# Kernel tuning notes

Hardware: AMD Instinct MI355X
Metric: run time of the kernel (lower is better)

## Reference

```python
import jax, jax.numpy as jnp
import numpy as np

B, S, D, L, R = 8, 128, 512, 512, 50  # batch, seq_len, input_dim, linear_dim, n_rel_labels


def _head_params(key, n_out):
    k1, k2, k3, k4 = jax.random.split(key, 4)
    s1 = 1.0 / np.sqrt(2 * D)
    s2 = 1.0 / np.sqrt(L)
    return (jax.random.uniform(k1, (2 * D, L), jnp.float32, -s1, s1),
            jax.random.uniform(k2, (L,), jnp.float32, -s1, s1),
            jax.random.uniform(k3, (L, n_out), jnp.float32, -s2, s2),
            jax.random.uniform(k4, (n_out,), jnp.float32, -s2, s2))


def setup_inputs() -> dict:
    key = jax.random.key(0)
    kx, ks, kh, kt, kl = jax.random.split(key, 5)
    x = jax.random.normal(kx, (B, S, D), jnp.float32)
    span = _head_params(ks, 1)
    h2h = _head_params(kh, 1)
    t2t = _head_params(kt, 1)
    lab = _head_params(kl, R)
    return {
        'x': x,
        'span_W1': span[0], 'span_b1': span[1], 'span_W2': span[2], 'span_b2': span[3],
        'h2h_W1': h2h[0], 'h2h_b1': h2h[1], 'h2h_W2': h2h[2], 'h2h_b2': h2h[3],
        't2t_W1': t2t[0], 't2t_b1': t2t[1], 't2t_W2': t2t[2], 't2t_b2': t2t[3],
        'lab_W1': lab[0], 'lab_b1': lab[1], 'lab_W2': lab[2], 'lab_b2': lab[3],
    }


def _pair_head(x, W1, b1, W2, b2):
    # Linear on concat([x_i, x_j]) == x_i @ W_left + x_j @ W_right  (avoids [B,S,S,2D] concat)
    d = x.shape[-1]
    Wl, Wr = W1[:d], W1[d:]
    left = jnp.einsum('bid,dl->bil', x, Wl)   # [B,S,L]
    right = jnp.einsum('bjd,dl->bjl', x, Wr)  # [B,S,L]
    h = jnp.tanh(left[:, :, None, :] + right[:, None, :, :] + b1)  # [B,S,S,L]
    return jnp.einsum('bijl,lo->bijo', h, W2) + b2  # [B,S,S,n_out]


def reference(x, span_W1, span_b1, span_W2, span_b2,
              h2h_W1, h2h_b1, h2h_W2, h2h_b2,
              t2t_W1, t2t_b1, t2t_W2, t2t_b2,
              lab_W1, lab_b1, lab_W2, lab_b2):
    shst = _pair_head(x, span_W1, span_b1, span_W2, span_b2)[..., 0]  # [B,S,S]
    # torch: movedim(-1,1) -> triu + triu(1).T -> movedim(1,-1)
    bt = jnp.swapaxes(shst, 1, 2)
    sym = jnp.triu(bt) + jnp.swapaxes(jnp.triu(bt, 1), -1, -2)
    shst = jnp.swapaxes(sym, 1, 2)
    shoh = _pair_head(x, h2h_W1, h2h_b1, h2h_W2, h2h_b2)[..., 0]
    stot = _pair_head(x, t2t_W1, t2t_b1, t2t_W2, t2t_b2)[..., 0]
    shoh_labels = _pair_head(x, lab_W1, lab_b1, lab_W2, lab_b2)  # [B,S,S,R]
    return (shst, shoh, stot, shoh_labels)
```

## Files before the change

### kernel.cpp

```cpp
#include <hip/hip_runtime.h>

#define Bsz 8
#define Ssz 128
#define Dsz 512
#define D2 1024
#define Lsz 512
#define Rsz 50
#define SLOT 524288
#define OUTMAT 131072

typedef __attribute__((ext_vector_type(8))) _Float16 f16x8;
typedef __attribute__((ext_vector_type(2))) __fp16 fp16x2;
typedef __attribute__((ext_vector_type(4))) float f32x4;

union UV4 { uint4 u; f16x8 h; };
union UH { unsigned short s; _Float16 h; };
union UP { fp16x2 h; unsigned u; };

struct K1Args {
  const float* W1[4];
  const float* b1[4];
};

__device__ __forceinline__ unsigned pkrtz(float a, float b) {
  UP c; c.h = __builtin_amdgcn_cvt_pkrtz(a, b); return c.u;
}
__device__ __forceinline__ unsigned short f2h(float v) {
  UH x; x.h = (_Float16)v; return x.s;
}
__device__ __forceinline__ float rcpf(float x) {
  return __builtin_amdgcn_rcpf(x);
}

__device__ __forceinline__ unsigned tanh2u(unsigned ea, unsigned eb) {
  UP a, b, p; a.u = ea; b.u = eb;
  const fp16x2 one = {(__fp16)1.0f, (__fp16)1.0f};
  p.h = a.h * b.h + one;
  const float h0 = fmaf(-2.0f, rcpf((float)p.h.x), 1.0f);
  const float h1 = fmaf(-2.0f, rcpf((float)p.h.y), 1.0f);
  return pkrtz(h0, h1);
}

__device__ __forceinline__ float d2(unsigned a, unsigned b, unsigned w,
                                    float acc) {
  UP pa, pb, pw, ps; pa.u = a; pb.u = b; pw.u = w;
  const fp16x2 one = {(__fp16)1.0f, (__fp16)1.0f};
  fp16x2 p = pa.h * pb.h + one;
  ps.u = pkrtz(rcpf((float)p.x), rcpf((float)p.y));
  return __builtin_amdgcn_fdot2(ps.h, pw.h, acc, false);
}

__global__ __launch_bounds__(256) void prep_all(
    const float* __restrict__ x, K1Args a, const float* __restrict__ W2,
    const float* __restrict__ w2a, const float* __restrict__ w2b,
    const float* __restrict__ w2c,
    const float* __restrict__ b2a, const float* __restrict__ b2b,
    const float* __restrict__ b2c,
    unsigned short* __restrict__ W1F, unsigned short* __restrict__ X16F,
    unsigned short* __restrict__ W2F, float* __restrict__ Sums) {
  const int z = blockIdx.z;
  const int t = threadIdx.x;
  if (z < 4) {
    if (blockIdx.x >= 8) return;
    __shared__ float S[64][65];
    const float* __restrict__ W = a.W1[z];
    const int n0 = blockIdx.x * 64;
    const int k0 = blockIdx.y * 64;
    {
      const int kk = t >> 2, c16 = (t & 3) * 16;
      const float* p = W + (k0 + kk) * Lsz + n0 + c16;
#pragma unroll
      for (int c = 0; c < 4; ++c) {
        float4 v = *(const float4*)(p + c * 4);
        S[kk][c16 + c * 4 + 0] = v.x; S[kk][c16 + c * 4 + 1] = v.y;
        S[kk][c16 + c * 4 + 2] = v.z; S[kk][c16 + c * 4 + 3] = v.w;
      }
    }
    __syncthreads();
#pragma unroll
    for (int o = t; o < 512; o += 256) {
      const int lane = o & 63;
      const int ntl = (o >> 6) & 3, kbl = o >> 8;
      const int n_l = ntl * 16 + (lane & 15);
      const int k_l = kbl * 32 + (lane >> 4) * 8;
      uint4 pk;
      pk.x = pkrtz(S[k_l + 0][n_l], S[k_l + 1][n_l]);
      pk.y = pkrtz(S[k_l + 2][n_l], S[k_l + 3][n_l]);
      pk.z = pkrtz(S[k_l + 4][n_l], S[k_l + 5][n_l]);
      pk.w = pkrtz(S[k_l + 6][n_l], S[k_l + 7][n_l]);
      const long addr =
          ((long)((z * 32 + blockIdx.x * 4 + ntl) * 32 + blockIdx.y * 2 + kbl) *
               64 + lane) * 8;
      *(uint4*)(W1F + addr) = pk;
    }
  } else if (z == 4) {
    if (blockIdx.x >= 16) return;
    const int idx = (blockIdx.y * 16 + blockIdx.x) * 256 + t;
    const int frag = idx >> 6, lane = idx & 63;
    const int m = (frag >> 4) * 16 + (lane & 15);
    const int k0 = (frag & 15) * 32 + (lane >> 4) * 8;
    const float* p = x + m * Dsz + k0;
    float4 v0 = *(const float4*)p, v1 = *(const float4*)(p + 4);
    uint4 pk = make_uint4(pkrtz(v0.x, v0.y), pkrtz(v0.z, v0.w),
                          pkrtz(v1.x, v1.y), pkrtz(v1.z, v1.w));
    *(uint4*)(X16F + (long)idx * 8) = pk;
  } else {
    if (blockIdx.y != 0) return;
    if (blockIdx.x < 16) {
      const int idx = blockIdx.x * 256 + t;
      const int frag = idx >> 6, lane = idx & 63;
      const int o = (frag >> 4) * 16 + (lane & 15);
      const int k0 = (frag & 15) * 32 + (lane >> 4) * 8;
      float v[8];
#pragma unroll
      for (int e = 0; e < 8; ++e)
        v[e] = (o < Rsz) ? W2[(k0 + e) * Rsz + o] : 0.0f;
      uint4 pk = make_uint4(pkrtz(v[0], v[1]), pkrtz(v[2], v[3]),
                            pkrtz(v[4], v[5]), pkrtz(v[6], v[7]));
      *(uint4*)(W2F + (long)idx * 8) = pk;
    } else if (blockIdx.x < 19) {
      const int h = blockIdx.x - 16;
      const float* __restrict__ w2 = (h == 0) ? w2a : (h == 1 ? w2b : w2c);
      const float bb = (h == 0) ? b2a[0] : (h == 1 ? b2b[0] : b2c[0]);
      __shared__ float red[256];
      red[t] = w2[t] + w2[t + 256];
      __syncthreads();
      for (int s = 128; s > 0; s >>= 1) {
        if (t < s) red[t] += red[t + s];
        __syncthreads();
      }
      if (t == 0) Sums[h] = red[0] + bb;
    }
  }
}

__global__ __launch_bounds__(256) void gemm_lr_f16f(
    const unsigned short* __restrict__ X16F,
    const unsigned short* __restrict__ W1F, K1Args a,
    unsigned short* __restrict__ U) {
  const int side = blockIdx.z;
  const int h = side >> 1, r = side & 1;
  const float* __restrict__ bias = a.b1[h];
  const int tid = threadIdx.x;
  const int w = tid >> 6, lane = tid & 63;
  const int lm = lane & 15, q = lane >> 4;
  const int mtb = blockIdx.y * 4 + (w & 1) * 2;
  const int ntb = blockIdx.x * 4 + (w >> 1) * 2;

  f32x4 acc[2][2];
#pragma unroll
  for (int mt = 0; mt < 2; ++mt)
#pragma unroll
    for (int nt = 0; nt < 2; ++nt) {
      acc[mt][nt].x = 0.f; acc[mt][nt].y = 0.f;
      acc[mt][nt].z = 0.f; acc[mt][nt].w = 0.f;
    }

  for (int kb = 0; kb < 16; ++kb) {
    UV4 af[2], bf[2];
#pragma unroll
    for (int mt = 0; mt < 2; ++mt)
      af[mt].u = *(const uint4*)(X16F +
          ((long)((mtb + mt) * 16 + kb) * 64 + lane) * 8);
#pragma unroll
    for (int nt = 0; nt < 2; ++nt)
      bf[nt].u = *(const uint4*)(W1F +
          ((long)((h * 32 + ntb + nt) * 32 + r * 16 + kb) * 64 + lane) * 8);
#pragma unroll
    for (int mt = 0; mt < 2; ++mt)
#pragma unroll
      for (int nt = 0; nt < 2; ++nt)
        acc[mt][nt] = __builtin_amdgcn_mfma_f32_16x16x32_f16(
            af[mt].h, bf[nt].h, acc[mt][nt], 0, 0, 0);
  }

  unsigned short* slot = U + side * SLOT;
#pragma unroll
  for (int nt = 0; nt < 2; ++nt) {
    const int n_out = (ntb + nt) * 16 + lm;
    const float bb = (r == 0) ? bias[n_out] : 0.0f;
#pragma unroll
    for (int mt = 0; mt < 2; ++mt) {
#pragma unroll
      for (int reg = 0; reg < 4; ++reg) {
        const int m_out = (mtb + mt) * 16 + q * 4 + reg;
        float v;
        if (reg == 0) v = acc[mt][nt].x;
        else if (reg == 1) v = acc[mt][nt].y;
        else if (reg == 2) v = acc[mt][nt].z;
        else v = acc[mt][nt].w;
        slot[m_out * Lsz + n_out] = f2h(__expf(2.0f * (v + bb)));
      }
    }
  }
}

__global__ __launch_bounds__(256) void pair_fused(
    const unsigned short* __restrict__ U,
    const unsigned short* __restrict__ W2F,
    const float* __restrict__ b2l,
    const float* __restrict__ w2a, const float* __restrict__ w2b,
    const float* __restrict__ w2c, const float* __restrict__ Sums,
    float* __restrict__ out) {
  __shared__ unsigned short As[2][16][68];
  __shared__ unsigned short Bs[2][32][68];
  __shared__ unsigned w2p[2][32];

  const int b = blockIdx.y;
  const int tid = threadIdx.x;
  const int w = tid >> 6, lane = tid & 63;
  const int lm = lane & 15, q = lane >> 4;

  if ((blockIdx.x & 1) == 0) {
    const int i = blockIdx.x >> 1;
    const int jb = w * 32;

    const unsigned short* __restrict__ Lrow =
        U + 6 * SLOT + (b * Ssz + i) * Lsz;
    const unsigned short* __restrict__ Rb0 = U + 7 * SLOT + (long)b * Ssz * Lsz;
    float* out3 = out + 3 * OUTMAT;

    const unsigned short* Lb = Lrow + q * 8;
    const unsigned short* R0 = Rb0 + (jb + lm) * Lsz + q * 8;
    const unsigned short* R1 = Rb0 + (jb + 16 + lm) * Lsz + q * 8;
    const unsigned short* Bb = W2F + lane * 8;

    f32x4 acc[2][4];
#pragma unroll
    for (int mt = 0; mt < 2; ++mt)
#pragma unroll
      for (int nt = 0; nt < 4; ++nt) {
        acc[mt][nt].x = 0.f; acc[mt][nt].y = 0.f;
        acc[mt][nt].z = 0.f; acc[mt][nt].w = 0.f;
      }

#pragma unroll 2
    for (int c = 0; c < 8; ++c) {
      const uint4 lf0 = *(const uint4*)(Lb + c * 64);
      const uint4 lf1 = *(const uint4*)(Lb + c * 64 + 32);
#pragma unroll
      for (int kbl = 0; kbl < 2; ++kbl) {
        const uint4 lf = kbl ? lf1 : lf0;
        UV4 bfr[4];
#pragma unroll
        for (int nt = 0; nt < 4; ++nt)
          bfr[nt].u =
              *(const uint4*)(Bb + (long)(nt * 16 + kbl + 2 * c) * 512);
#pragma unroll
        for (int mt = 0; mt < 2; ++mt) {
          const uint4 rv =
              *(const uint4*)((mt ? R1 : R0) + c * 64 + kbl * 32);
          UV4 A;
          A.u = make_uint4(tanh2u(lf.x, rv.x), tanh2u(lf.y, rv.y),
                           tanh2u(lf.z, rv.z), tanh2u(lf.w, rv.w));
#pragma unroll
          for (int nt = 0; nt < 4; ++nt)
            acc[mt][nt] = __builtin_amdgcn_mfma_f32_16x16x32_f16(
                A.h, bfr[nt].h, acc[mt][nt], 0, 0, 0);
        }
      }
    }

#pragma unroll
    for (int nt = 0; nt < 4; ++nt) {
      const int o = nt * 16 + lm;
      if (o >= Rsz) continue;
      const float bias = b2l[o];
#pragma unroll
      for (int mt = 0; mt < 2; ++mt) {
#pragma unroll
        for (int reg = 0; reg < 4; ++reg) {
          const int j = jb + mt * 16 + q * 4 + reg;
          const long base = ((long)((b * Ssz + i) * Ssz) + j) * Rsz;
          float v;
          if (reg == 0) v = acc[mt][nt].x;
          else if (reg == 1) v = acc[mt][nt].y;
          else if (reg == 2) v = acc[mt][nt].z;
          else v = acc[mt][nt].w;
          out3[base + o] = v + bias;
        }
      }
    }
  } else {
    const int s = blockIdx.x >> 1;
    if (s >= 96) return;
    const int h = s >> 5;
    const int r = s & 31;
    const int it = r >> 2, jt = r & 3;
    const int i0 = it * 16, j0 = jt * 32;
    if (h == 0 && i0 + 15 < j0) return;
    const int t = tid;
    const int tj = t & 31;
    const int th = t >> 5;
    const int iA = th * 2;

    const unsigned short* __restrict__ A =
        U + (2 * h) * SLOT + (long)(b * Ssz + i0) * Lsz;
    const unsigned short* __restrict__ Bt =
        U + (2 * h + 1) * SLOT + (long)(b * Ssz + j0) * Lsz;
    const float* __restrict__ w2 = (h == 0) ? w2a : (h == 1 ? w2b : w2c);

    const int srow = t >> 3;
    const int scol = (t & 7) * 8;
    const unsigned short* Ag = A + srow * Lsz + scol;
    const unsigned short* Bg = Bt + srow * Lsz + scol;

    float accA0 = 0.f, accB0 = 0.f, accA1 = 0.f, accB1 = 0.f;

    {
      uint4 ra, rb; unsigned rw = 0;
      if (t < 128) ra = *(const uint4*)(Ag);
      rb = *(const uint4*)(Bg);
      if (t < 32) rw = pkrtz(w2[2 * t], w2[2 * t + 1]);
      if (t < 128) *(uint4*)&As[0][srow][scol] = ra;
      *(uint4*)&Bs[0][srow][scol] = rb;
      if (t < 32) w2p[0][t] = rw;
    }
    __syncthreads();

#pragma unroll 1
    for (int c = 0; c < 8; ++c) {
      const int buf = c & 1;
      uint4 ra, rb; unsigned rw = 0;
      if (c < 7) {
        const int lc = (c + 1) * 64;
        if (t < 128) ra = *(const uint4*)(Ag + lc);
        rb = *(const uint4*)(Bg + lc);
        if (t < 32) rw = pkrtz(w2[lc + 2 * t], w2[lc + 2 * t + 1]);
      }
#pragma unroll
      for (int l = 0; l < 64; l += 4) {
        const uint2 av0 = *(const uint2*)&As[buf][iA][l];
        const uint2 av1 = *(const uint2*)&As[buf][iA + 1][l];
        const uint2 bv  = *(const uint2*)&Bs[buf][tj][l];
        const unsigned w0 = w2p[buf][l >> 1];
        const unsigned w1 = w2p[buf][(l >> 1) + 1];
        accA0 = d2(av0.x, bv.x, w0, accA0);
        accB0 = d2(av0.y, bv.y, w1, accB0);
        accA1 = d2(av1.x, bv.x, w0, accA1);
        accB1 = d2(av1.y, bv.y, w1, accB1);
      }
      if (c < 7) {
        const int nb = buf ^ 1;
        if (t < 128) *(uint4*)&As[nb][srow][scol] = ra;
        *(uint4*)&Bs[nb][srow][scol] = rb;
        if (t < 32) w2p[nb][t] = rw;
        __syncthreads();
      }
    }

    const float Sh = Sums[h];
    const float v0 = fmaf(-2.0f, accA0 + accB0, Sh);
    const float v1 = fmaf(-2.0f, accA1 + accB1, Sh);
    const int i = i0 + iA, j = j0 + tj;
    if (h == 0) {
      if (j <= i) {
        out[(b * Ssz + i) * Ssz + j] = v0;
        out[(b * Ssz + j) * Ssz + i] = v0;
      }
      if (j <= i + 1) {
        out[(b * Ssz + i + 1) * Ssz + j] = v1;
        out[(b * Ssz + j) * Ssz + (i + 1)] = v1;
      }
    } else {
      float* o = out + h * OUTMAT;
      o[(b * Ssz + i) * Ssz + j] = v0;
      o[(b * Ssz + i + 1) * Ssz + j] = v1;
    }
  }
}

extern "C" void kernel_launch(void* const* d_in, const int* in_sizes, int n_in,
                              void* d_out, int out_size, void* d_ws,
                              size_t ws_size, hipStream_t stream) {
  (void)in_sizes; (void)n_in; (void)out_size; (void)ws_size;
  const float* x = (const float*)d_in[0];
  K1Args a;
  a.W1[0] = (const float*)d_in[1];  a.b1[0] = (const float*)d_in[2];
  a.W1[1] = (const float*)d_in[5];  a.b1[1] = (const float*)d_in[6];
  a.W1[2] = (const float*)d_in[9];  a.b1[2] = (const float*)d_in[10];
  a.W1[3] = (const float*)d_in[13]; a.b1[3] = (const float*)d_in[14];
  const float* w2a = (const float*)d_in[3];
  const float* b2a = (const float*)d_in[4];
  const float* w2b = (const float*)d_in[7];
  const float* b2b = (const float*)d_in[8];
  const float* w2c = (const float*)d_in[11];
  const float* b2c = (const float*)d_in[12];
  const float* W2l = (const float*)d_in[15];
  const float* b2l = (const float*)d_in[16];
  float* out = (float*)d_out;

  unsigned short* U    = (unsigned short*)d_ws;
  unsigned short* W1F  = U + 8 * SLOT;
  unsigned short* X16F = U + 8 * SLOT + 4 * (Lsz * D2);
  unsigned short* W2F  = U + 8 * SLOT + 5 * (Lsz * D2);
  float* Sums = (float*)(W2F + 64 * Lsz);

  prep_all<<<dim3(19, 16, 6), 256, 0, stream>>>(
      x, a, W2l, w2a, w2b, w2c, b2a, b2b, b2c, W1F, X16F, W2F, Sums);
  gemm_lr_f16f<<<dim3(8, 16, 8), 256, 0, stream>>>(X16F, W1F, a, U);
  pair_fused<<<dim3(256, Bsz), 256, 0, stream>>>(
      U, W2F, b2l, w2a, w2b, w2c, Sums, out);
}
```

Before: 174.5 us.

## Split scalar pair heads over L into four atomic partials and use fp32 math

```diff
diff --git a/kernel.cpp b/kernel.cpp
--- a/kernel.cpp
+++ b/kernel.cpp
@@ -22,6 +22,12 @@
   const float* b1[4];
 };
 
+__device__ __forceinline__ float f16lo(unsigned u) {
+  UH x; x.s = (unsigned short)(u & 0xffffu); return (float)x.h;
+}
+__device__ __forceinline__ float f16hi(unsigned u) {
+  UH x; x.s = (unsigned short)(u >> 16); return (float)x.h;
+}
 __device__ __forceinline__ unsigned pkrtz(float a, float b) {
   UP c; c.h = __builtin_amdgcn_cvt_pkrtz(a, b); return c.u;
 }
@@ -41,15 +47,6 @@
   return pkrtz(h0, h1);
 }
 
-__device__ __forceinline__ float d2(unsigned a, unsigned b, unsigned w,
-                                    float acc) {
-  UP pa, pb, pw, ps; pa.u = a; pb.u = b; pw.u = w;
-  const fp16x2 one = {(__fp16)1.0f, (__fp16)1.0f};
-  fp16x2 p = pa.h * pb.h + one;
-  ps.u = pkrtz(rcpf((float)p.x), rcpf((float)p.y));
-  return __builtin_amdgcn_fdot2(ps.h, pw.h, acc, false);
-}
-
 __global__ __launch_bounds__(256) void prep_all(
     const float* __restrict__ x, K1Args a, const float* __restrict__ W2,
     const float* __restrict__ w2a, const float* __restrict__ w2b,
@@ -57,7 +54,8 @@
     const float* __restrict__ b2a, const float* __restrict__ b2b,
     const float* __restrict__ b2c,
     unsigned short* __restrict__ W1F, unsigned short* __restrict__ X16F,
-    unsigned short* __restrict__ W2F, float* __restrict__ Sums) {
+    unsigned short* __restrict__ W2F, float* __restrict__ Sums,
+    float* __restrict__ out) {
   const int z = blockIdx.z;
   const int t = threadIdx.x;
   if (z < 4) {
@@ -130,6 +128,13 @@
         __syncthreads();
       }
       if (t == 0) Sums[h] = red[0] + bb;
+    } else if (blockIdx.x < 43) {
+      const int zb = blockIdx.x - 19;
+      float* base = out + zb * 16384;
+      const float4 zz = make_float4(0.f, 0.f, 0.f, 0.f);
+#pragma unroll
+      for (int k = 0; k < 16; ++k)
+        *(float4*)(base + k * 1024 + t * 4) = zz;
     }
   }
 }
@@ -202,17 +207,18 @@
     const float* __restrict__ w2a, const float* __restrict__ w2b,
     const float* __restrict__ w2c, const float* __restrict__ Sums,
     float* __restrict__ out) {
-  __shared__ unsigned short As[2][16][68];
-  __shared__ unsigned short Bs[2][32][68];
-  __shared__ unsigned w2p[2][32];
+  __shared__ unsigned short As[16][66];
+  __shared__ unsigned short Bs[32][66];
+  __shared__ float w2s[64];
 
   const int b = blockIdx.y;
   const int tid = threadIdx.x;
-  const int w = tid >> 6, lane = tid & 63;
-  const int lm = lane & 15, q = lane >> 4;
-
-  if ((blockIdx.x & 1) == 0) {
-    const int i = blockIdx.x >> 1;
+  const int xr = blockIdx.x & 3;
+
+  if (xr == 0) {
+    const int i = blockIdx.x >> 2;
+    const int w = tid >> 6, lane = tid & 63;
+    const int lm = lane & 15, q = lane >> 4;
     const int jb = w * 32;
 
     const unsigned short* __restrict__ Lrow =
@@ -282,90 +288,79 @@
       }
     }
   } else {
-    const int s = blockIdx.x >> 1;
-    if (s >= 96) return;
-    const int h = s >> 5;
-    const int r = s & 31;
+    const int s = (blockIdx.x >> 2) * 3 + xr - 1;
+    const int t6 = s >> 2, lq = s & 3;
+    const int h = t6 >> 5;
+    const int r = t6 & 31;
     const int it = r >> 2, jt = r & 3;
     const int i0 = it * 16, j0 = jt * 32;
     if (h == 0 && i0 + 15 < j0) return;
     const int t = tid;
     const int tj = t & 31;
-    const int th = t >> 5;
-    const int iA = th * 2;
+    const int th2 = (t >> 5) * 2;
 
     const unsigned short* __restrict__ A =
         U + (2 * h) * SLOT + (long)(b * Ssz + i0) * Lsz;
     const unsigned short* __restrict__ Bt =
         U + (2 * h + 1) * SLOT + (long)(b * Ssz + j0) * Lsz;
     const float* __restrict__ w2 = (h == 0) ? w2a : (h == 1 ? w2b : w2c);
+    const int lb = lq * 128;
 
     const int srow = t >> 3;
-    const int scol = (t & 7) * 8;
-    const unsigned short* Ag = A + srow * Lsz + scol;
-    const unsigned short* Bg = Bt + srow * Lsz + scol;
-
-    float accA0 = 0.f, accB0 = 0.f, accA1 = 0.f, accB1 = 0.f;
-
-    {
-      uint4 ra, rb; unsigned rw = 0;
-      if (t < 128) ra = *(const uint4*)(Ag);
-      rb = *(const uint4*)(Bg);
-      if (t < 32) rw = pkrtz(w2[2 * t], w2[2 * t + 1]);
-      if (t < 128) *(uint4*)&As[0][srow][scol] = ra;
-      *(uint4*)&Bs[0][srow][scol] = rb;
-      if (t < 32) w2p[0][t] = rw;
-    }
-    __syncthreads();
-
-#pragma unroll 1
-    for (int c = 0; c < 8; ++c) {
-      const int buf = c & 1;
-      uint4 ra, rb; unsigned rw = 0;
-      if (c < 7) {
-        const int lc = (c + 1) * 64;
-        if (t < 128) ra = *(const uint4*)(Ag + lc);
-        rb = *(const uint4*)(Bg + lc);
-        if (t < 32) rw = pkrtz(w2[lc + 2 * t], w2[lc + 2 * t + 1]);
-      }
-#pragma unroll
-      for (int l = 0; l < 64; l += 4) {
-        const uint2 av0 = *(const uint2*)&As[buf][iA][l];
-        const uint2 av1 = *(const uint2*)&As[buf][iA + 1][l];
-        const uint2 bv  = *(const uint2*)&Bs[buf][tj][l];
-        const unsigned w0 = w2p[buf][l >> 1];
-        const unsigned w1 = w2p[buf][(l >> 1) + 1];
-        accA0 = d2(av0.x, bv.x, w0, accA0);
-        accB0 = d2(av0.y, bv.y, w1, accB0);
-        accA1 = d2(av1.x, bv.x, w0, accA1);
-        accB1 = d2(av1.y, bv.y, w1, accB1);
-      }
-      if (c < 7) {
-        const int nb = buf ^ 1;
-        if (t < 128) *(uint4*)&As[nb][srow][scol] = ra;
-        *(uint4*)&Bs[nb][srow][scol] = rb;
-        if (t < 32) w2p[nb][t] = rw;
-        __syncthreads();
-      }
-    }
-
-    const float Sh = Sums[h];
-    const float v0 = fmaf(-2.0f, accA0 + accB0, Sh);
-    const float v1 = fmaf(-2.0f, accA1 + accB1, Sh);
-    const int i = i0 + iA, j = j0 + tj;
+    const int sc8 = (t & 7) * 8;
+
+    float accE0 = 0.f, accO0 = 0.f, accE1 = 0.f, accO1 = 0.f;
+
+    for (int c = 0; c < 2; ++c) {
+      const int lo = lb + c * 64;
+      __syncthreads();
+      if (t < 128) {
+        const uint4 ra = *(const uint4*)(A + srow * Lsz + lo + sc8);
+        *(unsigned*)&As[srow][sc8 + 0] = ra.x;
+        *(unsigned*)&As[srow][sc8 + 2] = ra.y;
+        *(unsigned*)&As[srow][sc8 + 4] = ra.z;
+        *(unsigned*)&As[srow][sc8 + 6] = ra.w;
+      }
+      {
+        const uint4 rb = *(const uint4*)(Bt + srow * Lsz + lo + sc8);
+        *(unsigned*)&Bs[srow][sc8 + 0] = rb.x;
+        *(unsigned*)&Bs[srow][sc8 + 2] = rb.y;
+        *(unsigned*)&Bs[srow][sc8 + 4] = rb.z;
+        *(unsigned*)&Bs[srow][sc8 + 6] = rb.w;
+      }
+      if (t < 64) w2s[t] = w2[lo + t];
+      __syncthreads();
+#pragma unroll 4
+      for (int l = 0; l < 64; l += 2) {
+        const unsigned ua0 = *(const unsigned*)&As[th2][l];
+        const unsigned ua1 = *(const unsigned*)&As[th2 + 1][l];
+        const unsigned ub  = *(const unsigned*)&Bs[tj][l];
+        const float2 wv = *(const float2*)&w2s[l];
+        const float b0 = f16lo(ub), b1 = f16hi(ub);
+        accE0 = fmaf(wv.x, rcpf(fmaf(f16lo(ua0), b0, 1.0f)), accE0);
+        accO0 = fmaf(wv.y, rcpf(fmaf(f16hi(ua0), b1, 1.0f)), accO0);
+        accE1 = fmaf(wv.x, rcpf(fmaf(f16lo(ua1), b0, 1.0f)), accE1);
+        accO1 = fmaf(wv.y, rcpf(fmaf(f16hi(ua1), b1, 1.0f)), accO1);
+      }
+    }
+
+    const float base = (lq == 0) ? Sums[h] : 0.0f;
+    const float v0 = fmaf(-2.0f, accE0 + accO0, base);
+    const float v1 = fmaf(-2.0f, accE1 + accO1, base);
+    const int i = i0 + th2, j = j0 + tj;
     if (h == 0) {
       if (j <= i) {
-        out[(b * Ssz + i) * Ssz + j] = v0;
-        out[(b * Ssz + j) * Ssz + i] = v0;
+        atomicAdd(&out[(b * Ssz + i) * Ssz + j], v0);
+        if (j < i) atomicAdd(&out[(b * Ssz + j) * Ssz + i], v0);
       }
       if (j <= i + 1) {
-        out[(b * Ssz + i + 1) * Ssz + j] = v1;
-        out[(b * Ssz + j) * Ssz + (i + 1)] = v1;
+        atomicAdd(&out[(b * Ssz + i + 1) * Ssz + j], v1);
+        if (j < i + 1) atomicAdd(&out[(b * Ssz + j) * Ssz + (i + 1)], v1);
       }
     } else {
       float* o = out + h * OUTMAT;
-      o[(b * Ssz + i) * Ssz + j] = v0;
-      o[(b * Ssz + i + 1) * Ssz + j] = v1;
+      atomicAdd(&o[(b * Ssz + i) * Ssz + j], v0);
+      atomicAdd(&o[(b * Ssz + i + 1) * Ssz + j], v1);
     }
   }
 }
@@ -396,9 +391,9 @@
   unsigned short* W2F  = U + 8 * SLOT + 5 * (Lsz * D2);
   float* Sums = (float*)(W2F + 64 * Lsz);
 
-  prep_all<<<dim3(19, 16, 6), 256, 0, stream>>>(
-      x, a, W2l, w2a, w2b, w2c, b2a, b2b, b2c, W1F, X16F, W2F, Sums);
+  prep_all<<<dim3(43, 16, 6), 256, 0, stream>>>(
+      x, a, W2l, w2a, w2b, w2c, b2a, b2b, b2c, W1F, X16F, W2F, Sums, out);
   gemm_lr_f16f<<<dim3(8, 16, 8), 256, 0, stream>>>(X16F, W1F, a, U);
-  pair_fused<<<dim3(256, Bsz), 256, 0, stream>>>(
+  pair_fused<<<dim3(512, Bsz), 256, 0, stream>>>(
       U, W2F, b2l, w2a, w2b, w2c, Sums, out);
 }
```

Measured after the change: 215.6 us. 1.24x slower.
